# Kernel optimization log

Measured on AMD Instinct MI355X. Metric: run time of the kernel, lower is better.

Reference implementation:

```python
import jax, jax.numpy as jnp
import numpy as np
from math import sqrt

D_MODEL, D_COND, N_HEADS = 512, 768, 8
B, H, W, L_COND = 8, 64, 64, 256


def setup_inputs() -> dict:
    key = jax.random.key(0)
    ks = jax.random.split(key, 7)
    return {
        "image": jax.random.normal(ks[0], (B, D_MODEL, H, W), jnp.float32),
        "cond": jax.random.normal(ks[1], (B, L_COND, D_COND), jnp.float32),
        "attention_mask": jnp.zeros((B, H * W, L_COND), jnp.float32),
        "Wq": jax.random.normal(ks[2], (D_MODEL, D_MODEL), jnp.float32) * 0.02,
        "Wk": jax.random.normal(ks[3], (D_MODEL, D_COND), jnp.float32) * 0.02,
        "Wv": jax.random.normal(ks[4], (D_MODEL, D_COND), jnp.float32) * 0.02,
        "Wo": jax.random.normal(ks[5], (D_MODEL, D_MODEL), jnp.float32) * 0.02,
        "bo": jnp.zeros((D_MODEL,), jnp.float32),
    }


def reference(image, cond, attention_mask, Wq, Wk, Wv, Wo, bo):
    b, d, h, w = image.shape
    L = h * w
    n = N_HEADS
    dh = d // n
    scale = sqrt(dh)
    # b d h w -> b l d
    x = image.reshape(b, d, L).transpose(0, 2, 1)
    # projections (torch Linear: y = x @ W.T), split heads: b l (n dh) -> b n l dh
    q = (x @ Wq.T).reshape(b, L, n, dh).transpose(0, 2, 1, 3)
    k = (cond @ Wk.T).reshape(b, -1, n, dh).transpose(0, 2, 1, 3)
    v = (cond @ Wv.T).reshape(b, -1, n, dh).transpose(0, 2, 1, 3)
    attn = jnp.einsum("bnqd,bnkd->bnqk", q, k) / scale
    attn = attn + attention_mask[:, None]  # b 1 L L_cond
    p = jax.nn.softmax(attn, axis=-1)
    o = jnp.einsum("bnqk,bnkd->bnqd", p, v)  # b n L dh
    # b n (h w) dh -> b (n dh) h w
    o = o.transpose(0, 1, 3, 2).reshape(b, d, h, w)
    # 1x1 conv == per-pixel linear over channels
    out = jnp.einsum("oc,bchw->bohw", Wo, o) + bo[None, :, None, None]
    return out
```

## Files before the change

kernel.cpp:

```cpp
#include <hip/hip_runtime.h>

typedef __bf16 bf16x8 __attribute__((ext_vector_type(8)));
typedef float f32x4 __attribute__((ext_vector_type(4)));
typedef unsigned short ush;

#define DEV __device__ __forceinline__


DEV ush f2bf(float x){
  union { float f; unsigned u; } v; v.f = x;
  unsigned r = v.u + 0x7FFFu + ((v.u >> 16) & 1u);
  return (ush)(r >> 16);
}

DEV void gload_lds16(const ush* g, ush* l){
  __builtin_amdgcn_global_load_lds(
      (const __attribute__((address_space(1))) unsigned int*)g,
      (__attribute__((address_space(3))) unsigned int*)l, 16, 0, 0);
}

__global__ __launch_bounds__(256) void tc_kernel(const float* __restrict__ img, ush* __restrict__ xT){
  __shared__ float tile[32][33];
  const int b = blockIdx.z;
  const int l0 = blockIdx.x << 5, c0 = blockIdx.y << 5;
  const int tx = threadIdx.x & 31, ty = threadIdx.x >> 5;
  const float* src = img + ((size_t)b*512 + c0)*4096 + l0;
  #pragma unroll
  for (int i = 0; i < 32; i += 8) tile[ty+i][tx] = src[(size_t)(ty+i)*4096 + tx];
  __syncthreads();
  ush* dst = xT + ((size_t)b*4096 + l0)*512 + c0;
  #pragma unroll
  for (int i = 0; i < 32; i += 8) dst[(size_t)(ty+i)*512 + tx] = f2bf(tile[tx][ty+i]);
}

__global__ __launch_bounds__(256) void cvt_kernel(const float* c0,const float* c1,const float* c2,
                                                  const float* c3,const float* c4,
                                                  ush* o0, ush* o1, ush* o2, ush* o3, ush* o4){
  const int N0=1572864, N1=262144, N2=393216, N3=393216, N4=262144;
  const int stride = gridDim.x * blockDim.x;
  for (int i = blockIdx.x*blockDim.x + threadIdx.x; i < N0+N1+N2+N3+N4; i += stride){
    int j = i; const float* s; ush* d;
    if (j < N0){ s=c0; d=o0; }
    else { j-=N0; if (j<N1){s=c1;d=o1;}
      else { j-=N1; if (j<N2){s=c2;d=o2;}
        else { j-=N2; if (j<N3){s=c3;d=o3;} else { j-=N3; s=c4; d=o4; } } } }
    d[j] = f2bf(s[j]);
  }
}

DEV void gemm_core(const ush* __restrict__ Ag, long long a_row0, int lda,
                   const ush* __restrict__ Bg, long long b_row0, int ldb,
                   int K, ush* As, ush* Bs, f32x4 acc[4][4])
{
  const int t = threadIdx.x;
  const int lane = t & 63;
  const int wid = t >> 6, wr = wid >> 1, wc = wid & 1;
  #pragma unroll
  for (int mt=0;mt<4;mt++)
    #pragma unroll
    for (int nt=0;nt<4;nt++) acc[mt][nt] = f32x4{0.f,0.f,0.f,0.f};

  const int nk = K >> 6;
  for (int kt = 0; kt < nk; ++kt){
    const int k0 = kt << 6;
    #pragma unroll
    for (int r = 0; r < 4; ++r){
      int idx = (r<<8) + t;
      int row = idx >> 3, slot = idx & 7;
      gload_lds16(Ag + (a_row0 + row)*(long long)lda + k0 + ((slot ^ (row&7))<<3), As + idx*8);
    }
    #pragma unroll
    for (int r = 0; r < 4; ++r){
      int idx = (r<<8) + t;
      int row = idx >> 3, slot = idx & 7;
      gload_lds16(Bg + (b_row0 + row)*(long long)ldb + k0 + ((slot ^ (row&7))<<3), Bs + idx*8);
    }
    __syncthreads();
    #pragma unroll
    for (int kk = 0; kk < 2; ++kk){
      bf16x8 af[4], bfv[4];
      #pragma unroll
      for (int mt=0;mt<4;mt++){
        int row = (wr<<6) + (mt<<4) + (lane & 15);
        int byte = (row<<7) + (kk<<6) + ((lane>>4)<<4);
        byte ^= (row & 7) << 4;
        af[mt] = *(const bf16x8*)((const char*)As + byte);
      }
      #pragma unroll
      for (int nt=0;nt<4;nt++){
        int row = (wc<<6) + (nt<<4) + (lane & 15);
        int byte = (row<<7) + (kk<<6) + ((lane>>4)<<4);
        byte ^= (row & 7) << 4;
        bfv[nt] = *(const bf16x8*)((const char*)Bs + byte);
      }
      #pragma unroll
      for (int mt=0;mt<4;mt++)
        #pragma unroll
        for (int nt=0;nt<4;nt++)
          acc[mt][nt] = __builtin_amdgcn_mfma_f32_16x16x32_bf16(af[mt], bfv[nt], acc[mt][nt], 0,0,0);
    }
    __syncthreads();
  }
}

__global__ __launch_bounds__(256,2) void qproj_kernel(const ush* __restrict__ xT, const ush* __restrict__ Wqb,
                                                      ush* __restrict__ Qg){
  __shared__ ush As[8192], Bs[8192];
  f32x4 acc[4][4];
  const int nb = blockIdx.x & 3, mb = blockIdx.x >> 2;
  gemm_core(xT, (long long)mb*128, 512, Wqb, (long long)nb*128, 512, 512, As, Bs, acc);
  const int lane = threadIdx.x & 63, wid = threadIdx.x >> 6, wr = wid>>1, wc = wid&1;
  #pragma unroll
  for (int mt=0;mt<4;mt++)
    #pragma unroll
    for (int nt=0;nt<4;nt++)
      #pragma unroll
      for (int r=0;r<4;r++){
        int m = mb*128 + (wr<<6) + (mt<<4) + ((lane>>4)<<2) + r;
        int n = (nb<<7) + (wc<<6) + (nt<<4) + (lane&15);
        int bb = m >> 12, l = m & 4095, hh = n >> 6, dh = n & 63;
        Qg[(((size_t)(bb*8 + hh)*4096 + l)<<6) + dh] = f2bf(acc[mt][nt][r] * 0.125f);
      }
}

__global__ __launch_bounds__(256,2) void kvproj_kernel(const ush* __restrict__ cb, const ush* __restrict__ Wkb,
                                                       const ush* __restrict__ Wvb, ush* __restrict__ Kg,
                                                       ush* __restrict__ Vt){
  __shared__ ush As[8192], Bs[8192];
  f32x4 acc[4][4];
  const int which = blockIdx.z;
  const int nb = blockIdx.x & 3, mb = blockIdx.x >> 2;
  gemm_core(cb, (long long)mb*128, 768, which ? Wvb : Wkb, (long long)nb*128, 768, 768, As, Bs, acc);
  const int lane = threadIdx.x & 63, wid = threadIdx.x >> 6, wr = wid>>1, wc = wid&1;
  #pragma unroll
  for (int mt=0;mt<4;mt++)
    #pragma unroll
    for (int nt=0;nt<4;nt++)
      #pragma unroll
      for (int r=0;r<4;r++){
        int m = mb*128 + (wr<<6) + (mt<<4) + ((lane>>4)<<2) + r;
        int n = (nb<<7) + (wc<<6) + (nt<<4) + (lane&15);
        int bb = m >> 8, j = m & 255;
        ush val = f2bf(acc[mt][nt][r]);
        if (!which) Kg[(((size_t)(bb*256 + j))<<9) + n] = val;
        else { int hh = n>>6, dh = n&63; Vt[(((size_t)((bb*8+hh)*64 + dh))<<8) + j] = val; }
      }
}

__global__ __launch_bounds__(512,2) void attn_kernel(const ush* __restrict__ Qg, const ush* __restrict__ Kg,
                                                     const ush* __restrict__ Vg, const float* __restrict__ mask,
                                                     ush* __restrict__ Oc){
  extern __shared__ char smem[];
  ush* Ks = (ush*)smem;
  ush* Vs = (ush*)(smem + 32768);
  ush* Ps = (ush*)(smem + 65536);
  const int t = threadIdx.x, lane = t & 63, wid = t >> 6;
  const int qb = blockIdx.x, h = blockIdx.y, b = blockIdx.z;

  #pragma unroll
  for (int r = 0; r < 4; ++r){
    int idx = (r<<9) + t;
    int j = idx >> 3, slot = idx & 7;
    gload_lds16(Kg + ((size_t)(b*256 + j))*512 + h*64 + ((slot ^ (j&7))<<3), Ks + idx*8);
  }
  #pragma unroll
  for (int r = 0; r < 4; ++r){
    int idx = (r<<9) + t;
    int dh = idx >> 5, slot = idx & 31;
    gload_lds16(Vg + ((size_t)((b*8 + h)*64 + dh))*256 + ((((slot&7) ^ (dh&7)) | (slot&24))<<3), Vs + idx*8);
  }

  const int q0 = qb*256 + wid*32;
  bf16x8 qf[2][2];
  #pragma unroll
  for (int mt=0;mt<2;mt++)
    #pragma unroll
    for (int kk=0;kk<2;kk++)
      qf[mt][kk] = *(const bf16x8*)(Qg + (((size_t)(b*8+h)*4096 + q0 + mt*16 + (lane&15))<<6)
                                       + kk*32 + ((lane>>4)<<3));
  __syncthreads();

  ush* Pw = Ps + wid*4096;
  #pragma unroll
  for (int mt=0; mt<2; ++mt){
    f32x4 sacc[16];
    #pragma unroll
    for (int nt=0;nt<16;nt++) sacc[nt] = f32x4{0.f,0.f,0.f,0.f};

    #pragma unroll
    for (int kk=0;kk<2;kk++){
      #pragma unroll
      for (int nt=0;nt<16;nt++){
        int krow = (nt<<4) + (lane & 15);
        int byte = (krow<<7) + (kk<<6) + ((lane>>4)<<4);
        byte ^= (krow & 7) << 4;
        bf16x8 kf = *(const bf16x8*)((const char*)Ks + byte);
        sacc[nt] = __builtin_amdgcn_mfma_f32_16x16x32_bf16(qf[mt][kk], kf, sacc[nt], 0,0,0);
      }
    }

    const float* mrow = mask + ((size_t)b*4096 + q0 + mt*16 + ((lane>>4)<<2))*256 + (lane & 15);
    #pragma unroll
    for (int nt=0;nt<16;nt++)
      #pragma unroll
      for (int r=0;r<4;r++)
        sacc[nt][r] += mrow[(r<<8) + (nt<<4)];

    float mx[4], sm[4], rl[4];
    #pragma unroll
    for (int r=0;r<4;r++){
      float m = sacc[0][r];
      #pragma unroll
      for (int nt=1;nt<16;nt++) m = fmaxf(m, sacc[nt][r]);
      m = fmaxf(m, __shfl_xor(m, 1, 64));
      m = fmaxf(m, __shfl_xor(m, 2, 64));
      m = fmaxf(m, __shfl_xor(m, 4, 64));
      m = fmaxf(m, __shfl_xor(m, 8, 64));
      mx[r] = m; sm[r] = 0.f;
    }
    #pragma unroll
    for (int nt=0;nt<16;nt++)
      #pragma unroll
      for (int r=0;r<4;r++){
        float p = __expf(sacc[nt][r] - mx[r]);
        sacc[nt][r] = p; sm[r] += p;
      }
    #pragma unroll
    for (int r=0;r<4;r++){
      sm[r] += __shfl_xor(sm[r], 1, 64);
      sm[r] += __shfl_xor(sm[r], 2, 64);
      sm[r] += __shfl_xor(sm[r], 4, 64);
      sm[r] += __shfl_xor(sm[r], 8, 64);
      rl[r] = 1.f / sm[r];
    }

    #pragma unroll
    for (int nt=0;nt<16;nt++)
      #pragma unroll
      for (int r=0;r<4;r++){
        int qr = ((lane>>4)<<2) + r;
        int byte = (qr<<9) + (((nt<<4) + (lane&15))<<1);
        byte ^= (qr & 7) << 4;
        *(ush*)((char*)Pw + byte) = f2bf(sacc[nt][r]);
      }

    f32x4 oacc[4];
    #pragma unroll
    for (int nt=0;nt<4;nt++) oacc[nt] = f32x4{0.f,0.f,0.f,0.f};
    #pragma unroll
    for (int kc=0;kc<8;kc++){
      int qrow = lane & 15;
      int pbyte = (qrow<<9) + (kc<<6) + ((lane>>4)<<4);
      pbyte ^= (qrow & 7) << 4;
      bf16x8 pf = *(const bf16x8*)((const char*)Pw + pbyte);
      #pragma unroll
      for (int nt=0;nt<4;nt++){
        int dr = (nt<<4) + (lane & 15);
        int vbyte = (dr<<9) + (kc<<6) + ((lane>>4)<<4);
        vbyte ^= (dr & 7) << 4;
        bf16x8 vf = *(const bf16x8*)((const char*)Vs + vbyte);
        oacc[nt] = __builtin_amdgcn_mfma_f32_16x16x32_bf16(pf, vf, oacc[nt], 0,0,0);
      }
    }
    #pragma unroll
    for (int nt=0;nt<4;nt++)
      #pragma unroll
      for (int r=0;r<4;r++){
        int q = q0 + mt*16 + ((lane>>4)<<2) + r;
        Oc[(((size_t)b*4096 + q)<<9) + h*64 + (nt<<4) + (lane&15)] = f2bf(oacc[nt][r] * rl[r]);
      }
  }
}

__global__ __launch_bounds__(256,2) void oproj_kernel(const ush* __restrict__ Wob, const ush* __restrict__ Oc,
                                                      const float* __restrict__ bo, float* __restrict__ out){
  __shared__ ush As[8192], Bs[8192];
  f32x4 acc[4][4];
  const int bz = blockIdx.z;
  const int mb = blockIdx.x >> 5, nb = blockIdx.x & 31;
  gemm_core(Wob, (long long)mb*128, 512, Oc + (size_t)bz*4096*512, (long long)nb*128, 512, 512, As, Bs, acc);
  const int lane = threadIdx.x & 63, wid = threadIdx.x >> 6, wr = wid>>1, wc = wid&1;
  #pragma unroll
  for (int mt=0;mt<4;mt++)
    #pragma unroll
    for (int nt=0;nt<4;nt++){
      #pragma unroll
      for (int r=0;r<4;r++){
        int m = (mb<<7) + (wr<<6) + (mt<<4) + ((lane>>4)<<2) + r;
        int n = (nb<<7) + (wc<<6) + (nt<<4) + (lane&15);
        out[(((size_t)(bz*512 + m))<<12) + n] = acc[mt][nt][r] + bo[m];
      }
    }
}

extern "C" void kernel_launch(void* const* d_in, const int* in_sizes, int n_in,
                              void* d_out, int out_size, void* d_ws, size_t ws_size,
                              hipStream_t stream){
  const float* image = (const float*)d_in[0];
  const float* cond  = (const float*)d_in[1];
  const float* mask  = (const float*)d_in[2];
  const float* Wq    = (const float*)d_in[3];
  const float* Wk    = (const float*)d_in[4];
  const float* Wv    = (const float*)d_in[5];
  const float* Wo    = (const float*)d_in[6];
  const float* bo    = (const float*)d_in[7];
  float* out = (float*)d_out;

  char* ws = (char*)d_ws;
  ush* xT   = (ush*)(ws);
  ush* Oc   = xT;
  ush* Qg   = (ush*)(ws + 33554432);
  ush* cndb = (ush*)(ws + 67108864);
  ush* Kg   = (ush*)(ws + 70254592);
  ush* Vt   = (ush*)(ws + 72351744);
  ush* Wqb  = (ush*)(ws + 74448896);
  ush* Wkb  = (ush*)(ws + 74973184);
  ush* Wvb  = (ush*)(ws + 75759616);
  ush* Wob  = (ush*)(ws + 76546048);

  (void)hipFuncSetAttribute((const void*)attn_kernel,
                            hipFuncAttributeMaxDynamicSharedMemorySize, 131072);

  tc_kernel<<<dim3(128,16,8), 256, 0, stream>>>(image, xT);
  cvt_kernel<<<dim3(1024), 256, 0, stream>>>(cond, Wq, Wk, Wv, Wo, cndb, Wqb, Wkb, Wvb, Wob);
  qproj_kernel<<<dim3(1024), 256, 0, stream>>>(xT, Wqb, Qg);
  kvproj_kernel<<<dim3(64,1,2), 256, 0, stream>>>(cndb, Wkb, Wvb, Kg, Vt);
  attn_kernel<<<dim3(16,8,8), 512, 131072, stream>>>(Qg, Kg, Vt, mask, Oc);
  oproj_kernel<<<dim3(128,1,8), 256, 0, stream>>>(Wob, Oc, bo, out);
}
```

Baseline: 183.6 us.

## Keep softmax probabilities in registers via transposed S=K·Q^T MFMA layout

The attention kernel now computes S transposed (K as the A operand, Q as B), so each lane holds one query row's scores. Row max and sum need only two cross-lane shuffles, and the mask is read with float4 loads. P is converted to bf16 in registers and fed straight into 16x16x16 MFMAs against V, which removes the per-wave P scratch in LDS. LDS drops from 128KB to 64KB and launch bounds are raised to 4 blocks per CU, trading higher register pressure for more occupancy and no LDS round-trip.

```diff
diff --git a/kernel.cpp b/kernel.cpp
--- a/kernel.cpp
+++ b/kernel.cpp
@@ -2,6 +2,7 @@
 
 typedef __bf16 bf16x8 __attribute__((ext_vector_type(8)));
 typedef float f32x4 __attribute__((ext_vector_type(4)));
+typedef short s4 __attribute__((ext_vector_type(4)));
 typedef unsigned short ush;
 
 #define DEV __device__ __forceinline__
@@ -147,13 +148,12 @@
       }
 }
 
-__global__ __launch_bounds__(512,2) void attn_kernel(const ush* __restrict__ Qg, const ush* __restrict__ Kg,
+__global__ __launch_bounds__(512,4) void attn_kernel(const ush* __restrict__ Qg, const ush* __restrict__ Kg,
                                                      const ush* __restrict__ Vg, const float* __restrict__ mask,
                                                      ush* __restrict__ Oc){
   extern __shared__ char smem[];
   ush* Ks = (ush*)smem;
   ush* Vs = (ush*)(smem + 32768);
-  ush* Ps = (ush*)(smem + 65536);
   const int t = threadIdx.x, lane = t & 63, wid = t >> 6;
   const int qb = blockIdx.x, h = blockIdx.y, b = blockIdx.z;
 
@@ -169,106 +169,86 @@
     int dh = idx >> 5, slot = idx & 31;
     gload_lds16(Vg + ((size_t)((b*8 + h)*64 + dh))*256 + ((((slot&7) ^ (dh&7)) | (slot&24))<<3), Vs + idx*8);
   }
-
+  __syncthreads();
+
+  const int l15 = lane & 15, kg = lane >> 4;
   const int q0 = qb*256 + wid*32;
-  bf16x8 qf[2][2];
-  #pragma unroll
-  for (int mt=0;mt<2;mt++)
-    #pragma unroll
-    for (int kk=0;kk<2;kk++)
-      qf[mt][kk] = *(const bf16x8*)(Qg + (((size_t)(b*8+h)*4096 + q0 + mt*16 + (lane&15))<<6)
-                                       + kk*32 + ((lane>>4)<<3));
-  __syncthreads();
-
-  ush* Pw = Ps + wid*4096;
-  #pragma unroll
-  for (int mt=0; mt<2; ++mt){
+  const ush* Qbase = Qg + ((size_t)(b*8 + h)*4096)*64;
+
+  #pragma unroll
+  for (int mt = 0; mt < 2; ++mt){
+    const int qg = q0 + mt*16 + l15;
+    bf16x8 qf0 = *(const bf16x8*)(Qbase + (size_t)qg*64 + (kg<<3));
+    bf16x8 qf1 = *(const bf16x8*)(Qbase + (size_t)qg*64 + 32 + (kg<<3));
+
     f32x4 sacc[16];
     #pragma unroll
     for (int nt=0;nt<16;nt++) sacc[nt] = f32x4{0.f,0.f,0.f,0.f};
 
     #pragma unroll
-    for (int kk=0;kk<2;kk++){
-      #pragma unroll
-      for (int nt=0;nt<16;nt++){
-        int krow = (nt<<4) + (lane & 15);
-        int byte = (krow<<7) + (kk<<6) + ((lane>>4)<<4);
-        byte ^= (krow & 7) << 4;
-        bf16x8 kf = *(const bf16x8*)((const char*)Ks + byte);
-        sacc[nt] = __builtin_amdgcn_mfma_f32_16x16x32_bf16(qf[mt][kk], kf, sacc[nt], 0,0,0);
-      }
-    }
-
-    const float* mrow = mask + ((size_t)b*4096 + q0 + mt*16 + ((lane>>4)<<2))*256 + (lane & 15);
-    #pragma unroll
-    for (int nt=0;nt<16;nt++)
-      #pragma unroll
-      for (int r=0;r<4;r++)
-        sacc[nt][r] += mrow[(r<<8) + (nt<<4)];
-
-    float mx[4], sm[4], rl[4];
-    #pragma unroll
-    for (int r=0;r<4;r++){
-      float m = sacc[0][r];
-      #pragma unroll
-      for (int nt=1;nt<16;nt++) m = fmaxf(m, sacc[nt][r]);
-      m = fmaxf(m, __shfl_xor(m, 1, 64));
-      m = fmaxf(m, __shfl_xor(m, 2, 64));
-      m = fmaxf(m, __shfl_xor(m, 4, 64));
-      m = fmaxf(m, __shfl_xor(m, 8, 64));
-      mx[r] = m; sm[r] = 0.f;
-    }
-    #pragma unroll
-    for (int nt=0;nt<16;nt++)
-      #pragma unroll
-      for (int r=0;r<4;r++){
-        float p = __expf(sacc[nt][r] - mx[r]);
-        sacc[nt][r] = p; sm[r] += p;
-      }
-    #pragma unroll
-    for (int r=0;r<4;r++){
-      sm[r] += __shfl_xor(sm[r], 1, 64);
-      sm[r] += __shfl_xor(sm[r], 2, 64);
-      sm[r] += __shfl_xor(sm[r], 4, 64);
-      sm[r] += __shfl_xor(sm[r], 8, 64);
-      rl[r] = 1.f / sm[r];
-    }
-
-    #pragma unroll
-    for (int nt=0;nt<16;nt++)
-      #pragma unroll
-      for (int r=0;r<4;r++){
-        int qr = ((lane>>4)<<2) + r;
-        int byte = (qr<<9) + (((nt<<4) + (lane&15))<<1);
-        byte ^= (qr & 7) << 4;
-        *(ush*)((char*)Pw + byte) = f2bf(sacc[nt][r]);
-      }
+    for (int nt=0;nt<16;++nt){
+      int row = (nt<<4) + l15;
+      const char* kb = (const char*)Ks + (row<<7);
+      int sw = (row&7)<<4;
+      bf16x8 kf0 = *(const bf16x8*)(kb + (((kg<<4)      ) ^ sw));
+      bf16x8 kf1 = *(const bf16x8*)(kb + (((kg<<4) + 64 ) ^ sw));
+      sacc[nt] = __builtin_amdgcn_mfma_f32_16x16x32_bf16(kf0, qf0, sacc[nt], 0,0,0);
+      sacc[nt] = __builtin_amdgcn_mfma_f32_16x16x32_bf16(kf1, qf1, sacc[nt], 0,0,0);
+    }
+
+    const float* mrow = mask + ((size_t)b*4096 + qg)*256 + (kg<<2);
+    #pragma unroll
+    for (int nt=0;nt<16;++nt){
+      float4 mv = *(const float4*)(mrow + (nt<<4));
+      sacc[nt][0] += mv.x; sacc[nt][1] += mv.y; sacc[nt][2] += mv.z; sacc[nt][3] += mv.w;
+    }
+
+    float mx = sacc[0][0];
+    #pragma unroll
+    for (int nt=0;nt<16;++nt)
+      #pragma unroll
+      for (int r=0;r<4;++r) mx = fmaxf(mx, sacc[nt][r]);
+    mx = fmaxf(mx, __shfl_xor(mx, 16, 64));
+    mx = fmaxf(mx, __shfl_xor(mx, 32, 64));
+    float sm = 0.f;
+    #pragma unroll
+    for (int nt=0;nt<16;++nt)
+      #pragma unroll
+      for (int r=0;r<4;++r){
+        float p = __expf(sacc[nt][r] - mx);
+        sacc[nt][r] = p; sm += p;
+      }
+    sm += __shfl_xor(sm, 16, 64);
+    sm += __shfl_xor(sm, 32, 64);
+    const float rl = 1.f / sm;
+
+    s4 pf[16];
+    #pragma unroll
+    for (int nt=0;nt<16;++nt)
+      #pragma unroll
+      for (int r=0;r<4;++r) pf[nt][r] = (short)f2bf(sacc[nt][r]);
 
     f32x4 oacc[4];
     #pragma unroll
-    for (int nt=0;nt<4;nt++) oacc[nt] = f32x4{0.f,0.f,0.f,0.f};
-    #pragma unroll
-    for (int kc=0;kc<8;kc++){
-      int qrow = lane & 15;
-      int pbyte = (qrow<<9) + (kc<<6) + ((lane>>4)<<4);
-      pbyte ^= (qrow & 7) << 4;
-      bf16x8 pf = *(const bf16x8*)((const char*)Pw + pbyte);
-      #pragma unroll
-      for (int nt=0;nt<4;nt++){
-        int dr = (nt<<4) + (lane & 15);
-        int vbyte = (dr<<9) + (kc<<6) + ((lane>>4)<<4);
-        vbyte ^= (dr & 7) << 4;
-        bf16x8 vf = *(const bf16x8*)((const char*)Vs + vbyte);
-        oacc[nt] = __builtin_amdgcn_mfma_f32_16x16x32_bf16(pf, vf, oacc[nt], 0,0,0);
-      }
-    }
-    #pragma unroll
-    for (int nt=0;nt<4;nt++)
-      #pragma unroll
-      for (int r=0;r<4;r++){
-        int q = q0 + mt*16 + ((lane>>4)<<2) + r;
-        Oc[(((size_t)b*4096 + q)<<9) + h*64 + (nt<<4) + (lane&15)] = f2bf(oacc[nt][r] * rl[r]);
-      }
+    for (int tl=0;tl<4;++tl) oacc[tl] = f32x4{0.f,0.f,0.f,0.f};
+    #pragma unroll
+    for (int nt=0;nt<16;++nt){
+      #pragma unroll
+      for (int tl=0;tl<4;++tl){
+        int dh = (tl<<4) + l15;
+        int off = ((nt<<5) + (kg<<3)) ^ ((dh&7)<<4);
+        s4 vf = *(const s4*)((const char*)Vs + (dh<<9) + off);
+        oacc[tl] = __builtin_amdgcn_mfma_f32_16x16x16bf16_1k(vf, pf[nt], oacc[tl], 0,0,0);
+      }
+    }
+
+    #pragma unroll
+    for (int tl=0;tl<4;++tl){
+      s4 ov;
+      #pragma unroll
+      for (int r=0;r<4;++r) ov[r] = (short)f2bf(oacc[tl][r] * rl);
+      *(s4*)(Oc + (((size_t)b*4096 + qg)<<9) + h*64 + (tl<<4) + (kg<<2)) = ov;
+    }
   }
 }
 
@@ -319,12 +299,12 @@
   ush* Wob  = (ush*)(ws + 76546048);
 
   (void)hipFuncSetAttribute((const void*)attn_kernel,
-                            hipFuncAttributeMaxDynamicSharedMemorySize, 131072);
+                            hipFuncAttributeMaxDynamicSharedMemorySize, 65536);
 
   tc_kernel<<<dim3(128,16,8), 256, 0, stream>>>(image, xT);
   cvt_kernel<<<dim3(1024), 256, 0, stream>>>(cond, Wq, Wk, Wv, Wo, cndb, Wqb, Wkb, Wvb, Wob);
   qproj_kernel<<<dim3(1024), 256, 0, stream>>>(xT, Wqb, Qg);
   kvproj_kernel<<<dim3(64,1,2), 256, 0, stream>>>(cndb, Wkb, Wvb, Kg, Vt);
-  attn_kernel<<<dim3(16,8,8), 512, 131072, stream>>>(Qg, Kg, Vt, mask, Oc);
+  attn_kernel<<<dim3(16,8,8), 512, 65536, stream>>>(Qg, Kg, Vt, mask, Oc);
   oproj_kernel<<<dim3(128,1,8), 256, 0, stream>>>(Wob, Oc, bo, out);
 }
```

Result: slower. 320.4 us (+74.5%).
